# Performance work log

Hardware: AMD Instinct MI355X
Metric: run time of the kernel (lower is better)

Reference implementation:

```python
import jax, jax.numpy as jnp
import numpy as np

N = 100000      # nodes
E = 1600000     # edges (before self-loops)
DIM = 128       # input feature dim
H = 5           # attention heads
C = 10          # per-head output channels
G = 256         # graphs in batch
NEG_SLOPE = 0.2 # PyG GATConv default


def setup_inputs() -> dict:
    key = jax.random.key(0)
    ks = jax.random.split(key, 8)
    x = jax.random.normal(ks[0], (N, DIM), jnp.float32)
    edge_index = jax.random.randint(ks[1], (2, E), 0, N, dtype=jnp.int64)
    batch = jnp.sort(jax.random.randint(ks[2], (N,), 0, G, dtype=jnp.int64))
    W = jax.random.normal(ks[3], (DIM, H * C), jnp.float32) * 0.05
    att_src = jax.random.normal(ks[4], (H, C), jnp.float32) * 0.1
    att_dst = jax.random.normal(ks[5], (H, C), jnp.float32) * 0.1
    bias = jnp.zeros((H * C,), jnp.float32)
    lin_w = jax.random.normal(ks[6], (H * C, 1), jnp.float32) * 0.1
    lin_b = jnp.zeros((1,), jnp.float32)
    return {"x": x, "W": W, "att_src": att_src, "att_dst": att_dst,
            "bias": bias, "lin_w": lin_w, "lin_b": lin_b,
            "edge_index": edge_index, "batch": batch}


def reference(x, W, att_src, att_dst, bias, lin_w, lin_b, edge_index, batch):
    n = x.shape[0]
    # PyG GATConv adds self-loops by default
    loop = jnp.arange(n, dtype=edge_index.dtype)
    src = jnp.concatenate([edge_index[0], loop])  # message sources j
    dst = jnp.concatenate([edge_index[1], loop])  # message targets i

    xw = (x @ W).reshape(n, H, C)                       # [N,H,C]
    a_src = jnp.einsum('nhc,hc->nh', xw, att_src)       # [N,H]
    a_dst = jnp.einsum('nhc,hc->nh', xw, att_dst)       # [N,H]

    logits = jax.nn.leaky_relu(a_src[src] + a_dst[dst], NEG_SLOPE)  # [Etot,H]
    # segment softmax over incoming edges per target node
    m = jax.ops.segment_max(logits, dst, num_segments=n)
    ex = jnp.exp(logits - m[dst])
    denom = jax.ops.segment_sum(ex, dst, num_segments=n)
    alpha = ex / denom[dst]                              # [Etot,H]

    msg = alpha[:, :, None] * xw[src]                    # [Etot,H,C]
    out = jax.ops.segment_sum(msg, dst, num_segments=n).reshape(n, H * C) + bias
    out = jax.nn.elu(out)                                # [N,H*C]

    # global_mean_pool over graph ids
    gsum = jax.ops.segment_sum(out, batch, num_segments=G)
    cnt = jax.ops.segment_sum(jnp.ones((n,), out.dtype), batch, num_segments=G)
    h = gsum / jnp.maximum(cnt, 1.0)[:, None]            # [G,H*C]

    # dropout p=0.5 is identity at inference (training=False)
    y = jax.nn.sigmoid(h @ lin_w + lin_b)                # [G,1]
    return (h, y)
```

## Files before the change

kernel.cpp:

```cpp
#include <hip/hip_runtime.h>
#include <hip/hip_bf16.h>
#include <hip/hip_fp8.h>
#include <math.h>

#define DIM 128
#define H 5
#define C 10
#define HC 50
#define NG 256
#define NEG_SLOPE 0.2f
#define UNR 8
#define WP 136
#define LOG2E 1.4426950408889634f

#define BSH 6
#define NB 1563
#define SB_CAP 1344
#define B1_BLOCKS 196
#define B1_CHUNK 8192

#define BKN2 32
#define ROWS_LDS2 (BKN2 * 64)

typedef short short8 __attribute__((ext_vector_type(8)));
typedef float floatx4 __attribute__((ext_vector_type(4)));
typedef float floatx2 __attribute__((ext_vector_type(2)));

__device__ inline short f2bf(float f) {
  __hip_bfloat16 h = __float2bfloat16(f);
  return *reinterpret_cast<short*>(&h);
}
#if __has_builtin(__builtin_amdgcn_cvt_f32_fp8)
__device__ inline float fp8tof(int b) { return __builtin_amdgcn_cvt_f32_fp8(b, 0); }
#else
__device__ inline float fp8tof(int b) {
  __hip_fp8_e4m3 v;
  v.__x = (__hip_fp8_storage_t)b;
  return (float)v;
}
#endif
#if __has_builtin(__builtin_amdgcn_cvt_pk_f32_fp8)
__device__ inline floatx2 fp8pk2(int us) {
  return __builtin_amdgcn_cvt_pk_f32_fp8(us, false);
}
#else
__device__ inline floatx2 fp8pk2(int us) {
  floatx2 r;
  r.x = fp8tof(us & 0xff);
  r.y = fp8tof((us >> 8) & 0xff);
  return r;
}
#endif
#if __has_builtin(__builtin_amdgcn_exp2f)
__device__ inline float fexp2(float x) { return __builtin_amdgcn_exp2f(x); }
#else
__device__ inline float fexp2(float x) { return exp2f(x); }
#endif
#if __has_builtin(__builtin_amdgcn_cvt_pk_fp8_f32)
__device__ inline unsigned ftofp8pk(float a, float b) {
  return (unsigned)__builtin_amdgcn_cvt_pk_fp8_f32(a, b, 0, false) & 0xffffu;
}
__device__ inline unsigned char ftofp8(float f) {
  return (unsigned char)(ftofp8pk(f, f) & 0xff);
}
#else
__device__ inline unsigned char ftofp8(float f) {
  __hip_fp8_e4m3 v(f);
  return v.__x;
}
__device__ inline unsigned ftofp8pk(float a, float b) {
  return (unsigned)ftofp8(a) | ((unsigned)ftofp8(b) << 8);
}
#endif

__global__ void k_zero(int* __restrict__ g) {
  int t = blockIdx.x * blockDim.x + threadIdx.x;
  if (t < NB) g[t] = 0;
}

__global__ __launch_bounds__(256) void k_split(
    const int* __restrict__ src, const int* __restrict__ dst,
    int* __restrict__ gcur, int* __restrict__ seg,
    const float* __restrict__ W, const float* __restrict__ att_src,
    const float* __restrict__ att_dst, short* __restrict__ swt_g,
    unsigned char* __restrict__ recb, int E_, int n) {
  __shared__ int hist[NB], curs[NB], baser[NB];
  int tid = threadIdx.x;
  if (blockIdx.x == B1_BLOCKS) {
    if (tid < 64) recb[((size_t)n << 6) + tid] = (tid < HC) ? 0x00 : 0xFE;
    for (int idx = tid; idx < HC * 128; idx += 256) {
      int j = idx >> 7, k = idx & 127;
      swt_g[idx] = f2bf(W[k * HC + j]);
    }
    if (tid < 128) {
      float sv[H] = {0.f, 0.f, 0.f, 0.f, 0.f};
      float dv[H] = {0.f, 0.f, 0.f, 0.f, 0.f};
#pragma unroll
      for (int c = 0; c < HC; ++c) {
        float w = W[tid * HC + c];
        sv[c / C] += w * att_src[c];
        dv[c / C] += w * att_dst[c];
      }
#pragma unroll
      for (int h = 0; h < H; ++h) {
        swt_g[(HC + h) * 128 + tid] = f2bf(sv[h] * LOG2E);
        swt_g[(55 + h) * 128 + tid] = f2bf(dv[h] * LOG2E);
      }
    } else {
      int k = tid - 128;
      for (int j = 60; j < 64; ++j) swt_g[j * 128 + k] = 0;
    }
    return;
  }
  for (int i = tid; i < NB; i += 256) hist[i] = 0;
  __syncthreads();
  int e0 = blockIdx.x * B1_CHUNK;
  int dreg[32];
#pragma unroll
  for (int k = 0; k < 32; ++k) {
    int e = e0 + (k << 8) + tid;
    dreg[k] = (e < E_) ? dst[e] : -1;
    if (dreg[k] >= 0) atomicAdd(&hist[((unsigned)dreg[k]) >> BSH], 1);
  }
  __syncthreads();
  for (int i = tid; i < NB; i += 256) {
    baser[i] = hist[i] ? atomicAdd(&gcur[i], hist[i]) : 0;
    curs[i] = 0;
  }
  __syncthreads();
#pragma unroll
  for (int k = 0; k < 32; ++k) {
    if (dreg[k] >= 0) {
      int d = dreg[k];
      int s = ((unsigned)d) >> BSH;
      int pos = baser[s] + atomicAdd(&curs[s], 1);
      if (pos < SB_CAP)
        seg[(size_t)s * SB_CAP + pos] = (src[e0 + (k << 8) + tid] << 6) | (d & 63);
    }
  }
}

__global__ __launch_bounds__(256) void k_mfma(
    const float* __restrict__ x, const short* __restrict__ swt_g,
    unsigned char* __restrict__ recb, __hip_bfloat16* __restrict__ adst, int n) {
  __shared__ short swt[64 * WP];
  for (int idx = threadIdx.x; idx < 1024; idx += 256) {
    int row = idx >> 4;
    *(short8*)&swt[row * WP + (idx & 15) * 8] = *(const short8*)(swt_g + idx * 8);
  }
  __syncthreads();
  int wv = threadIdx.x >> 6, lane = threadIdx.x & 63;
  int tiles = (n + 15) >> 4;
  int tile = blockIdx.x * 4 + wv;
  if (tile >= tiles) return;
  int r = lane & 15, q = lane >> 4;
  int node = tile * 16 + r;
  const float* xr = x + (size_t)min(node, n - 1) * DIM + q * 8;
  floatx4 acc[4];
#pragma unroll
  for (int nt = 0; nt < 4; ++nt) acc[nt] = (floatx4){0.f, 0.f, 0.f, 0.f};
#pragma unroll
  for (int ks = 0; ks < 4; ++ks) {
    float4 a0 = *(const float4*)(xr + ks * 32);
    float4 a1 = *(const float4*)(xr + ks * 32 + 4);
    short8 bx;
    bx[0] = f2bf(a0.x); bx[1] = f2bf(a0.y); bx[2] = f2bf(a0.z); bx[3] = f2bf(a0.w);
    bx[4] = f2bf(a1.x); bx[5] = f2bf(a1.y); bx[6] = f2bf(a1.z); bx[7] = f2bf(a1.w);
    const short* wb = &swt[r * WP + q * 8 + ks * 32];
    short8 w0 = *(const short8*)(wb);
    short8 w1 = *(const short8*)(wb + 16 * WP);
    short8 w2 = *(const short8*)(wb + 32 * WP);
    short8 w3 = *(const short8*)(wb + 48 * WP);
    acc[0] = __builtin_amdgcn_mfma_f32_16x16x32_bf16(w0, bx, acc[0], 0, 0, 0);
    acc[1] = __builtin_amdgcn_mfma_f32_16x16x32_bf16(w1, bx, acc[1], 0, 0, 0);
    acc[2] = __builtin_amdgcn_mfma_f32_16x16x32_bf16(w2, bx, acc[2], 0, 0, 0);
    acc[3] = __builtin_amdgcn_mfma_f32_16x16x32_bf16(w3, bx, acc[3], 0, 0, 0);
  }
  float xa = __shfl_up(acc[3][3], 16);
  float xb = __shfl_up(acc[3][1], 16);
  float xc = __shfl_up(acc[3][2], 16);
  if (node < n) {
    size_t base = (size_t)node << 6;
#pragma unroll
    for (int nt = 0; nt < 3; ++nt) {
      unsigned d = ftofp8pk(acc[nt][0], acc[nt][1]) |
                   (ftofp8pk(acc[nt][2], acc[nt][3]) << 16);
      *(unsigned*)(recb + base + nt * 16 + (q << 2)) = d;
    }
    unsigned d;
    if (q == 0) {
      d = ftofp8pk(acc[3][0], acc[3][1]) | (ftofp8pk(acc[3][2], acc[3][2]) << 16);
    } else if (q == 1) {
      d = ftofp8pk(xa, xa) | (ftofp8pk(acc[3][0], acc[3][0]) << 16);
      adst[(size_t)node * H + 0] = __float2bfloat16(acc[3][3]);
    } else if (q == 2) {
      d = ftofp8pk(xb, xb) | (ftofp8pk(xc, xc) << 16);
      adst[(size_t)node * H + 1] = __float2bfloat16(acc[3][0]);
      adst[(size_t)node * H + 2] = __float2bfloat16(acc[3][1]);
      adst[(size_t)node * H + 3] = __float2bfloat16(acc[3][2]);
      adst[(size_t)node * H + 4] = __float2bfloat16(acc[3][3]);
    } else {
      d = 0;
    }
    *(unsigned*)(recb + base + 48 + (q << 2)) = d;
  }
}

__global__ __launch_bounds__(256) void k_bin_gat(
    const int* __restrict__ seg, const int* __restrict__ gcur,
    const unsigned char* __restrict__ recb, const __hip_bfloat16* __restrict__ adst,
    const float* __restrict__ bias, float* __restrict__ out_node, int n, int par) {
  __shared__ int rows[ROWS_LDS2];
  __shared__ __align__(16) int wbuf[4][128];
  int tid = threadIdx.x;
  int blk = blockIdx.x * 2 + par;
  int b = blk >> 1;
  int half32 = blk & 1;
  int lo = (b << BSH) + (half32 << 5);
  int hi = min(lo + BKN2, n);
  for (int k = tid; k < ROWS_LDS2; k += 256) rows[k] = n;
  __syncthreads();
  int cnt = min(gcur[b], SB_CAP);
  for (int k = tid; k < cnt; k += 256) {
    int e = seg[(size_t)b * SB_CAP + k];
    int dl = e & 63;
    if ((dl >> 5) == half32) {
      int s = ((unsigned)e) >> 6;
      int base = (dl & 31) << 6;
      int off = s & 63;
      int old = atomicExch(&rows[base + off], s);
      int probes = 0;
      while (old != n && probes < 128) {
        off = (off + 1) & 63;
        old = atomicExch(&rows[base + off], old);
        ++probes;
      }
    }
  }
  __syncthreads();

  int w = tid >> 6, lane = tid & 63;
  int* wb = wbuf[w];
  int nn = hi - lo;
  int pairsN = (nn + 1) >> 1;
  int hl = lane & 31;
  int hf = lane >> 5;
  bool chl = hl < 25;
  int h = hl / 5;
  int bpidx = ((hf << 5) + 25 + h) << 2;
  unsigned rowoff = (unsigned)(hl << 1);
  int rbase = hf << 6;

  for (int pr = w; pr < pairsN; pr += 4) {
    int i0l = pr * 2;
    int i1l = min(i0l + 1, nn - 1);
    int i0 = lo + i0l, i1 = lo + i1l;
    int iown = hf ? i1 : i0;
    float adi = 0.f;
    if (chl) adi = __bfloat162float(adst[(size_t)iown * H + h]);

    int jraw0 = rows[(i0l << 6) | lane];
    int jraw1 = rows[(i1l << 6) | lane];
    ((int2*)wb)[lane] = make_int2(n, n);
    bool v0 = (unsigned)jraw0 < (unsigned)n;
    unsigned long long mk0 = __ballot(v0);
    int deg0 = __popcll(mk0);
    int bel0 = __popcll(mk0 & ((1ull << lane) - 1ull));
    if (v0) wb[bel0] = jraw0;
    bool v1 = (unsigned)jraw1 < (unsigned)n;
    unsigned long long mk1 = __ballot(v1);
    int deg1 = __popcll(mk1);
    int bel1 = __popcll(mk1 & ((1ull << lane) - 1ull));
    if (v1) wb[64 + bel1] = jraw1;
    int mx = max(deg0, deg1);

    float dpA, dpB = 0.f, a0A, a0B = 0.f, a1A, a1B = 0.f;
    {
      int us = *(const unsigned short*)(recb + (((size_t)(unsigned)iown << 6) | rowoff));
      int asv = __builtin_amdgcn_ds_bpermute(bpidx, us);
      float asi = fp8tof(asv);
      float z = asi + adi;
      z = fmaxf(z, NEG_SLOPE * z);
      float pw = fexp2(z);
      floatx2 f = fp8pk2(us);
      dpA = pw;
      a0A = pw * f.x;
      a1A = pw * f.y;
    }
    for (int s0 = 0; s0 < mx; s0 += UNR) {
      int2 jp[UNR / 2];
#pragma unroll
      for (int up = 0; up < UNR / 2; ++up)
        jp[up] = *(const int2*)&wb[rbase + s0 + up * 2];
#pragma unroll
      for (int u = 0; u < UNR; ++u) {
        unsigned j = (unsigned)((u & 1) ? jp[u >> 1].y : jp[u >> 1].x);
        int us = *(const unsigned short*)(recb + (((size_t)j << 6) | rowoff));
        int asv = __builtin_amdgcn_ds_bpermute(bpidx, us);
        float asi = fp8tof(asv);
        float z = asi + adi;
        z = fmaxf(z, NEG_SLOPE * z);
        float pw = fexp2(z);
        floatx2 f = fp8pk2(us);
        if (u & 1) {
          dpB += pw;
          a0B = fmaf(pw, f.x, a0B);
          a1B = fmaf(pw, f.y, a1B);
        } else {
          dpA += pw;
          a0A = fmaf(pw, f.x, a0A);
          a1A = fmaf(pw, f.y, a1A);
        }
      }
    }
    if (chl) {
      float dp = dpA + dpB;
      float a0 = a0A + a0B, a1 = a1A + a1B;
      int c0 = hl * 2;
      float o0 = a0 / dp + bias[c0];
      o0 = o0 > 0.f ? o0 : __expf(o0) - 1.f;
      float o1 = a1 / dp + bias[c0 + 1];
      o1 = o1 > 0.f ? o1 : __expf(o1) - 1.f;
      float2 st;
      st.x = o0;
      st.y = o1;
      *(float2*)(out_node + (size_t)iown * HC + c0) = st;
    }
  }
}

__global__ __launch_bounds__(1024) void k_pool(
    const float* __restrict__ out_node, const int* __restrict__ batch,
    const float* __restrict__ lin_w, const float* __restrict__ lin_b,
    float* __restrict__ out, int n) {
  __shared__ int sb[2];
  __shared__ float sacc[16][HC];
  int g = blockIdx.x;
  int t = threadIdx.x;
  if (t < 2) {
    int target = g + t, lo = 0, hi = n;
    while (lo < hi) {
      int mid = (lo + hi) >> 1;
      if (batch[mid] < target) lo = mid + 1; else hi = mid;
    }
    sb[t] = lo;
  }
  __syncthreads();
  int s = sb[0], e = sb[1];
  int w = t >> 6, lane = t & 63;
  float a = 0.f;
  if (lane < HC)
    for (int i = s + w; i < e; i += 16) a += out_node[(size_t)i * HC + lane];
  if (lane < HC) sacc[w][lane] = a;
  __syncthreads();
  if (t < HC) {
    float r0 = 0.f, r1 = 0.f, r2 = 0.f, r3 = 0.f;
#pragma unroll
    for (int k = 0; k < 4; ++k) {
      r0 += sacc[k][t];
      r1 += sacc[4 + k][t];
      r2 += sacc[8 + k][t];
      r3 += sacc[12 + k][t];
    }
    float hv = ((r0 + r1) + (r2 + r3)) / fmaxf((float)(e - s), 1.f);
    out[g * HC + t] = hv;
    sacc[0][t] = hv * lin_w[t];
  }
  __syncthreads();
  if (t == 0) {
    float p = 0.f;
    for (int c = 0; c < HC; ++c) p += sacc[0][c];
    out[NG * HC + g] = 1.f / (1.f + __expf(-(p + lin_b[0])));
  }
}

extern "C" void kernel_launch(void* const* d_in, const int* in_sizes, int n_in,
                              void* d_out, int out_size, void* d_ws, size_t ws_size,
                              hipStream_t stream) {
  const float* x       = (const float*)d_in[0];
  const float* W       = (const float*)d_in[1];
  const float* att_src = (const float*)d_in[2];
  const float* att_dst = (const float*)d_in[3];
  const float* bias    = (const float*)d_in[4];
  const float* lin_w   = (const float*)d_in[5];
  const float* lin_b   = (const float*)d_in[6];
  const int*   eidx    = (const int*)d_in[7];
  const int*   batch   = (const int*)d_in[8];

  int n  = in_sizes[0] / DIM;
  int E_ = in_sizes[7] / 2;
  const int* srcp = eidx;
  const int* dstp = eidx + E_;

  char* p = (char*)d_ws;
  float* out_node = (float*)p; p += (size_t)n * HC * sizeof(float);
  unsigned char* recb = (unsigned char*)p; p += (size_t)(n + 1) * 64;
  __hip_bfloat16* adst = (__hip_bfloat16*)p; p += (size_t)n * H * sizeof(__hip_bfloat16);
  p = (char*)(((uintptr_t)p + 255) & ~(uintptr_t)255);
  short* swt_g = (short*)p; p += 64 * 128 * sizeof(short);
  p = (char*)(((uintptr_t)p + 255) & ~(uintptr_t)255);
  int* gcur = (int*)p; p += NB * sizeof(int);
  p = (char*)(((uintptr_t)p + 255) & ~(uintptr_t)255);
  int* seg = (int*)p; p += (size_t)NB * SB_CAP * sizeof(int);

  float* out = (float*)d_out;

  int tiles = (n + 15) / 16;
  int mfma_blocks = (tiles + 3) / 4;
  int nbk2 = (n + BKN2 - 1) / BKN2;

  k_zero<<<2, 1024, 0, stream>>>(gcur);
  k_split<<<B1_BLOCKS + 1, 256, 0, stream>>>(
      srcp, dstp, gcur, seg, W, att_src, att_dst, swt_g, recb, E_, n);
  k_mfma<<<mfma_blocks, 256, 0, stream>>>(x, swt_g, recb, adst, n);
  k_bin_gat<<<(nbk2 + 1) / 2, 256, 0, stream>>>(
      seg, gcur, recb, adst, bias, out_node, n, 0);
  k_bin_gat<<<nbk2 / 2, 256, 0, stream>>>(
      seg, gcur, recb, adst, bias, out_node, n, 1);
  k_pool<<<NG, 1024, 0, stream>>>(out_node, batch, lin_w, lin_b, out, n);
}
```

Baseline: 206.3 us.

## Replace LDS histogram binning with padded global atomics and merge GAT launches

The edge-binning kernel drops its per-block shared-memory histogram, prefix and scatter passes. Each edge now does a direct global atomicAdd on a per-bucket counter padded to 16 ints, to avoid false sharing, and it runs in a grid-stride loop over 2048 blocks. The two parity-split k_bin_gat launches are merged into one launch covering all blocks. This removes LDS setup, block barriers and one launch, but sends about 1.6M global atomics to 1563 hot counters, which may contend heavily.

```diff
diff --git a/kernel.cpp b/kernel.cpp
--- a/kernel.cpp
+++ b/kernel.cpp
@@ -16,8 +16,8 @@
 #define BSH 6
 #define NB 1563
 #define SB_CAP 1344
-#define B1_BLOCKS 196
-#define B1_CHUNK 8192
+#define GPAD 16
+#define SPLIT_BLOCKS 2048
 
 #define BKN2 32
 #define ROWS_LDS2 (BKN2 * 64)
@@ -75,7 +75,7 @@
 
 __global__ void k_zero(int* __restrict__ g) {
   int t = blockIdx.x * blockDim.x + threadIdx.x;
-  if (t < NB) g[t] = 0;
+  if (t < NB * GPAD) g[t] = 0;
 }
 
 __global__ __launch_bounds__(256) void k_split(
@@ -84,9 +84,8 @@
     const float* __restrict__ W, const float* __restrict__ att_src,
     const float* __restrict__ att_dst, short* __restrict__ swt_g,
     unsigned char* __restrict__ recb, int E_, int n) {
-  __shared__ int hist[NB], curs[NB], baser[NB];
   int tid = threadIdx.x;
-  if (blockIdx.x == B1_BLOCKS) {
+  if (blockIdx.x == SPLIT_BLOCKS) {
     if (tid < 64) recb[((size_t)n << 6) + tid] = (tid < HC) ? 0x00 : 0xFE;
     for (int idx = tid; idx < HC * 128; idx += 256) {
       int j = idx >> 7, k = idx & 127;
@@ -112,31 +111,13 @@
     }
     return;
   }
-  for (int i = tid; i < NB; i += 256) hist[i] = 0;
-  __syncthreads();
-  int e0 = blockIdx.x * B1_CHUNK;
-  int dreg[32];
-#pragma unroll
-  for (int k = 0; k < 32; ++k) {
-    int e = e0 + (k << 8) + tid;
-    dreg[k] = (e < E_) ? dst[e] : -1;
-    if (dreg[k] >= 0) atomicAdd(&hist[((unsigned)dreg[k]) >> BSH], 1);
-  }
-  __syncthreads();
-  for (int i = tid; i < NB; i += 256) {
-    baser[i] = hist[i] ? atomicAdd(&gcur[i], hist[i]) : 0;
-    curs[i] = 0;
-  }
-  __syncthreads();
-#pragma unroll
-  for (int k = 0; k < 32; ++k) {
-    if (dreg[k] >= 0) {
-      int d = dreg[k];
-      int s = ((unsigned)d) >> BSH;
-      int pos = baser[s] + atomicAdd(&curs[s], 1);
-      if (pos < SB_CAP)
-        seg[(size_t)s * SB_CAP + pos] = (src[e0 + (k << 8) + tid] << 6) | (d & 63);
-    }
+  int stride = SPLIT_BLOCKS * 256;
+  for (int e = blockIdx.x * 256 + tid; e < E_; e += stride) {
+    int d = dst[e];
+    int ent = (src[e] << 6) | (d & 63);
+    int s = ((unsigned)d) >> BSH;
+    int pos = atomicAdd(&gcur[s * GPAD], 1);
+    if (pos < SB_CAP) seg[(size_t)s * SB_CAP + pos] = ent;
   }
 }
 
@@ -209,18 +190,18 @@
 __global__ __launch_bounds__(256) void k_bin_gat(
     const int* __restrict__ seg, const int* __restrict__ gcur,
     const unsigned char* __restrict__ recb, const __hip_bfloat16* __restrict__ adst,
-    const float* __restrict__ bias, float* __restrict__ out_node, int n, int par) {
+    const float* __restrict__ bias, float* __restrict__ out_node, int n) {
   __shared__ int rows[ROWS_LDS2];
   __shared__ __align__(16) int wbuf[4][128];
   int tid = threadIdx.x;
-  int blk = blockIdx.x * 2 + par;
+  int blk = blockIdx.x;
   int b = blk >> 1;
   int half32 = blk & 1;
   int lo = (b << BSH) + (half32 << 5);
   int hi = min(lo + BKN2, n);
   for (int k = tid; k < ROWS_LDS2; k += 256) rows[k] = n;
   __syncthreads();
-  int cnt = min(gcur[b], SB_CAP);
+  int cnt = min(gcur[b * GPAD], SB_CAP);
   for (int k = tid; k < cnt; k += 256) {
     int e = seg[(size_t)b * SB_CAP + k];
     int dl = e & 63;
@@ -399,7 +380,7 @@
   p = (char*)(((uintptr_t)p + 255) & ~(uintptr_t)255);
   short* swt_g = (short*)p; p += 64 * 128 * sizeof(short);
   p = (char*)(((uintptr_t)p + 255) & ~(uintptr_t)255);
-  int* gcur = (int*)p; p += NB * sizeof(int);
+  int* gcur = (int*)p; p += (size_t)NB * GPAD * sizeof(int);
   p = (char*)(((uintptr_t)p + 255) & ~(uintptr_t)255);
   int* seg = (int*)p; p += (size_t)NB * SB_CAP * sizeof(int);
 
@@ -409,13 +390,10 @@
   int mfma_blocks = (tiles + 3) / 4;
   int nbk2 = (n + BKN2 - 1) / BKN2;
 
-  k_zero<<<2, 1024, 0, stream>>>(gcur);
-  k_split<<<B1_BLOCKS + 1, 256, 0, stream>>>(
+  k_zero<<<(NB * GPAD + 1023) / 1024, 1024, 0, stream>>>(gcur);
+  k_split<<<SPLIT_BLOCKS + 1, 256, 0, stream>>>(
       srcp, dstp, gcur, seg, W, att_src, att_dst, swt_g, recb, E_, n);
   k_mfma<<<mfma_blocks, 256, 0, stream>>>(x, swt_g, recb, adst, n);
-  k_bin_gat<<<(nbk2 + 1) / 2, 256, 0, stream>>>(
-      seg, gcur, recb, adst, bias, out_node, n, 0);
-  k_bin_gat<<<nbk2 / 2, 256, 0, stream>>>(
-      seg, gcur, recb, adst, bias, out_node, n, 1);
+  k_bin_gat<<<nbk2, 256, 0, stream>>>(seg, gcur, recb, adst, bias, out_node, n);
   k_pool<<<NG, 1024, 0, stream>>>(out_node, batch, lin_w, lin_b, out, n);
 }
```

Result: slower. 279.3 us (+35.4%).

## Fuse edge bucketing and MFMA projection into one launch; merge bin_gat launches

Applied to the files above, without the earlier changes.

Merges the edge-split kernel and the MFMA node-projection kernel into a single launch, with block ranges choosing the role. Each MFMA block now builds the bf16 weight tile in LDS from W directly instead of reading a precomputed global copy. The sentinel record write moves into the zero kernel. The two parity-split bin_gat launches become one. This removes several launches and lets the two independent phases overlap, but every MFMA block now recomputes the weight prep, and the shared LDS allocation sized for the histogram (about 18.7 KB) may reduce occupancy for the MFMA blocks.

```diff
diff --git a/kernel.cpp b/kernel.cpp
--- a/kernel.cpp
+++ b/kernel.cpp
@@ -73,85 +73,81 @@
 }
 #endif
 
-__global__ void k_zero(int* __restrict__ g) {
+__global__ void k_zero(int* __restrict__ g, unsigned char* __restrict__ recb,
+                       int n) {
   int t = blockIdx.x * blockDim.x + threadIdx.x;
   if (t < NB) g[t] = 0;
-}
-
-__global__ __launch_bounds__(256) void k_split(
+  if (blockIdx.x == 1 && threadIdx.x < 64)
+    recb[((size_t)n << 6) + threadIdx.x] = (threadIdx.x < HC) ? 0x00 : 0xFE;
+}
+
+__global__ __launch_bounds__(256) void k_work(
     const int* __restrict__ src, const int* __restrict__ dst,
     int* __restrict__ gcur, int* __restrict__ seg,
-    const float* __restrict__ W, const float* __restrict__ att_src,
-    const float* __restrict__ att_dst, short* __restrict__ swt_g,
-    unsigned char* __restrict__ recb, int E_, int n) {
-  __shared__ int hist[NB], curs[NB], baser[NB];
+    const float* __restrict__ x, const float* __restrict__ W,
+    const float* __restrict__ att_src, const float* __restrict__ att_dst,
+    unsigned char* __restrict__ recb, __hip_bfloat16* __restrict__ adst,
+    int E_, int n) {
+  __shared__ __align__(16) char smem[NB * 3 * sizeof(int)];
   int tid = threadIdx.x;
-  if (blockIdx.x == B1_BLOCKS) {
-    if (tid < 64) recb[((size_t)n << 6) + tid] = (tid < HC) ? 0x00 : 0xFE;
-    for (int idx = tid; idx < HC * 128; idx += 256) {
-      int j = idx >> 7, k = idx & 127;
-      swt_g[idx] = f2bf(W[k * HC + j]);
-    }
+  if (blockIdx.x < B1_BLOCKS) {
+    int* hist = (int*)smem;
+    int* curs = hist + NB;
+    int* baser = curs + NB;
+    for (int i = tid; i < NB; i += 256) hist[i] = 0;
+    __syncthreads();
+    int e0 = blockIdx.x * B1_CHUNK;
+    int dreg[32];
+#pragma unroll
+    for (int k = 0; k < 32; ++k) {
+      int e = e0 + (k << 8) + tid;
+      dreg[k] = (e < E_) ? dst[e] : -1;
+      if (dreg[k] >= 0) atomicAdd(&hist[((unsigned)dreg[k]) >> BSH], 1);
+    }
+    __syncthreads();
+    for (int i = tid; i < NB; i += 256) {
+      baser[i] = hist[i] ? atomicAdd(&gcur[i], hist[i]) : 0;
+      curs[i] = 0;
+    }
+    __syncthreads();
+#pragma unroll
+    for (int k = 0; k < 32; ++k) {
+      if (dreg[k] >= 0) {
+        int d = dreg[k];
+        int s = ((unsigned)d) >> BSH;
+        int pos = baser[s] + atomicAdd(&curs[s], 1);
+        if (pos < SB_CAP)
+          seg[(size_t)s * SB_CAP + pos] = (src[e0 + (k << 8) + tid] << 6) | (d & 63);
+      }
+    }
+    return;
+  }
+  short* swt = (short*)smem;
+  {
+    int k = tid & 127;
     if (tid < 128) {
+      for (int j = 0; j < HC; ++j) swt[j * WP + k] = f2bf(W[k * HC + j]);
+    } else {
       float sv[H] = {0.f, 0.f, 0.f, 0.f, 0.f};
       float dv[H] = {0.f, 0.f, 0.f, 0.f, 0.f};
 #pragma unroll
       for (int c = 0; c < HC; ++c) {
-        float w = W[tid * HC + c];
+        float w = W[k * HC + c];
         sv[c / C] += w * att_src[c];
         dv[c / C] += w * att_dst[c];
       }
 #pragma unroll
       for (int h = 0; h < H; ++h) {
-        swt_g[(HC + h) * 128 + tid] = f2bf(sv[h] * LOG2E);
-        swt_g[(55 + h) * 128 + tid] = f2bf(dv[h] * LOG2E);
+        swt[(HC + h) * WP + k] = f2bf(sv[h] * LOG2E);
+        swt[(55 + h) * WP + k] = f2bf(dv[h] * LOG2E);
       }
-    } else {
-      int k = tid - 128;
-      for (int j = 60; j < 64; ++j) swt_g[j * 128 + k] = 0;
-    }
-    return;
-  }
-  for (int i = tid; i < NB; i += 256) hist[i] = 0;
-  __syncthreads();
-  int e0 = blockIdx.x * B1_CHUNK;
-  int dreg[32];
-#pragma unroll
-  for (int k = 0; k < 32; ++k) {
-    int e = e0 + (k << 8) + tid;
-    dreg[k] = (e < E_) ? dst[e] : -1;
-    if (dreg[k] >= 0) atomicAdd(&hist[((unsigned)dreg[k]) >> BSH], 1);
-  }
-  __syncthreads();
-  for (int i = tid; i < NB; i += 256) {
-    baser[i] = hist[i] ? atomicAdd(&gcur[i], hist[i]) : 0;
-    curs[i] = 0;
-  }
-  __syncthreads();
-#pragma unroll
-  for (int k = 0; k < 32; ++k) {
-    if (dreg[k] >= 0) {
-      int d = dreg[k];
-      int s = ((unsigned)d) >> BSH;
-      int pos = baser[s] + atomicAdd(&curs[s], 1);
-      if (pos < SB_CAP)
-        seg[(size_t)s * SB_CAP + pos] = (src[e0 + (k << 8) + tid] << 6) | (d & 63);
-    }
-  }
-}
-
-__global__ __launch_bounds__(256) void k_mfma(
-    const float* __restrict__ x, const short* __restrict__ swt_g,
-    unsigned char* __restrict__ recb, __hip_bfloat16* __restrict__ adst, int n) {
-  __shared__ short swt[64 * WP];
-  for (int idx = threadIdx.x; idx < 1024; idx += 256) {
-    int row = idx >> 4;
-    *(short8*)&swt[row * WP + (idx & 15) * 8] = *(const short8*)(swt_g + idx * 8);
-  }
-  __syncthreads();
-  int wv = threadIdx.x >> 6, lane = threadIdx.x & 63;
+      for (int j = 60; j < 64; ++j) swt[j * WP + k] = 0;
+    }
+  }
+  __syncthreads();
+  int wv = tid >> 6, lane = tid & 63;
   int tiles = (n + 15) >> 4;
-  int tile = blockIdx.x * 4 + wv;
+  int tile = (blockIdx.x - B1_BLOCKS) * 4 + wv;
   if (tile >= tiles) return;
   int r = lane & 15, q = lane >> 4;
   int node = tile * 16 + r;
@@ -209,11 +205,11 @@
 __global__ __launch_bounds__(256) void k_bin_gat(
     const int* __restrict__ seg, const int* __restrict__ gcur,
     const unsigned char* __restrict__ recb, const __hip_bfloat16* __restrict__ adst,
-    const float* __restrict__ bias, float* __restrict__ out_node, int n, int par) {
+    const float* __restrict__ bias, float* __restrict__ out_node, int n) {
   __shared__ int rows[ROWS_LDS2];
   __shared__ __align__(16) int wbuf[4][128];
   int tid = threadIdx.x;
-  int blk = blockIdx.x * 2 + par;
+  int blk = blockIdx.x;
   int b = blk >> 1;
   int half32 = blk & 1;
   int lo = (b << BSH) + (half32 << 5);
@@ -397,8 +393,6 @@
   unsigned char* recb = (unsigned char*)p; p += (size_t)(n + 1) * 64;
   __hip_bfloat16* adst = (__hip_bfloat16*)p; p += (size_t)n * H * sizeof(__hip_bfloat16);
   p = (char*)(((uintptr_t)p + 255) & ~(uintptr_t)255);
-  short* swt_g = (short*)p; p += 64 * 128 * sizeof(short);
-  p = (char*)(((uintptr_t)p + 255) & ~(uintptr_t)255);
   int* gcur = (int*)p; p += NB * sizeof(int);
   p = (char*)(((uintptr_t)p + 255) & ~(uintptr_t)255);
   int* seg = (int*)p; p += (size_t)NB * SB_CAP * sizeof(int);
@@ -409,13 +403,9 @@
   int mfma_blocks = (tiles + 3) / 4;
   int nbk2 = (n + BKN2 - 1) / BKN2;
 
-  k_zero<<<2, 1024, 0, stream>>>(gcur);
-  k_split<<<B1_BLOCKS + 1, 256, 0, stream>>>(
-      srcp, dstp, gcur, seg, W, att_src, att_dst, swt_g, recb, E_, n);
-  k_mfma<<<mfma_blocks, 256, 0, stream>>>(x, swt_g, recb, adst, n);
-  k_bin_gat<<<(nbk2 + 1) / 2, 256, 0, stream>>>(
-      seg, gcur, recb, adst, bias, out_node, n, 0);
-  k_bin_gat<<<nbk2 / 2, 256, 0, stream>>>(
-      seg, gcur, recb, adst, bias, out_node, n, 1);
+  k_zero<<<2, 1024, 0, stream>>>(gcur, recb, n);
+  k_work<<<B1_BLOCKS + mfma_blocks, 256, 0, stream>>>(
+      srcp, dstp, gcur, seg, x, W, att_src, att_dst, recb, adst, E_, n);
+  k_bin_gat<<<nbk2, 256, 0, stream>>>(seg, gcur, recb, adst, bias, out_node, n);
   k_pool<<<NG, 1024, 0, stream>>>(out_node, batch, lin_w, lin_b, out, n);
 }
```

After: 200.6 us. -2.8%, faster.
